# Kernel optimization log

Hardware: AMD Instinct MI355X
Metric: run time of the kernel (lower is better)

The kernel has to match this reference:

```python
import jax, jax.numpy as jnp
import numpy as np

HEADS = 16
EMBED = 1024


def setup_inputs() -> dict:
    key = jax.random.key(0)
    k1, k2, k3, k4, k5, k6 = jax.random.split(key, 6)
    N, S, E = 2, 2048, EMBED
    return {
        "values": jax.random.normal(k1, (N, S, E), dtype=jnp.float32),
        "keys": jax.random.normal(k2, (N, S, E), dtype=jnp.float32),
        "query": jax.random.normal(k3, (N, S, E), dtype=jnp.float32),
        "mask": jax.random.randint(k4, (N, 1, S, S), 0, 2, dtype=jnp.int32),
        "W_out": jax.random.normal(k5, (E, E), dtype=jnp.float32) * 0.02,
        "b_out": jax.random.normal(k6, (E,), dtype=jnp.float32) * 0.02,
    }


def reference(values, keys, query, mask, W_out, b_out):
    N, Q, E = query.shape
    K = keys.shape[1]
    H = HEADS
    D = E // H
    v = values.reshape(N, K, H, D)
    k = keys.reshape(N, K, H, D)
    q = query.reshape(N, Q, H, D)
    # [N, H, Q, K] score matrix (faithful to the naive einsum formulation)
    energy = jnp.einsum("nqhd,nkhd->nhqk", q, k)
    energy = jnp.where(mask == 0, jnp.float32(-1e20), energy)
    # NOTE: original scales by sqrt(embed_size), not sqrt(head_dim)
    attention = jax.nn.softmax(energy / jnp.sqrt(jnp.float32(E)), axis=3)
    out = jnp.einsum("nhqk,nkhd->nqhd", attention, v).reshape(N, Q, E)
    return out @ W_out.T + b_out
```

## Files before the change

kernel.cpp:

```cpp
#include <hip/hip_runtime.h>
#include <hip/hip_bf16.h>


#define S_LEN  2048
#define EMB    1024
#define NHEAD  16
#define DHEAD  64
#define NBATCH 2

#define KSC 0.04508422002778011f

typedef float              f32x4    __attribute__((ext_vector_type(4)));
typedef float              f32x16   __attribute__((ext_vector_type(16)));
typedef __bf16             bf16x8   __attribute__((ext_vector_type(8)));
typedef unsigned short     ushort8v __attribute__((ext_vector_type(8)));
typedef unsigned long long u64;

union FragU { ushort8v u; bf16x8 b; };
union BFrag { unsigned u32[4]; bf16x8 b; };

__device__ __forceinline__ unsigned short f2b(float f) {
  union { __hip_bfloat16 h; unsigned short u; } c;
  c.h = __float2bfloat16(f);
  return c.u;
}

__device__ __forceinline__ unsigned int cvt_pk_bf16(float lo, float hi) {
  unsigned int r;
  asm("v_cvt_pk_bf16_f32 %0, %1, %2" : "=v"(r) : "v"(lo), "v"(hi));
  return r;
}

#define PSWAP(a, b) asm("v_permlane32_swap_b32 %0, %1" : "+v"(a), "+v"(b))

#define GLD16(g, l)                                                            \
  __builtin_amdgcn_global_load_lds(                                            \
      (__attribute__((address_space(1))) void*)(g),                            \
      (__attribute__((address_space(3))) void*)(l), 16, 0, 0)

__global__ __launch_bounds__(256) void prep(
    const float* __restrict__ Wo, unsigned short* __restrict__ Wb,
    const float* __restrict__ Kg, unsigned short* __restrict__ Kb,
    const float* __restrict__ Vg, unsigned short* __restrict__ Vt,
    const int* __restrict__ Mg,   u64* __restrict__ Mb)
{
  const int bid = blockIdx.x;
  const int tid = threadIdx.x;
  if (bid < 2560) {
    const float* X = (bid < 512) ? Wo : Kg;
    unsigned short* Y = (bid < 512) ? Wb : Kb;
    const int bb = (bid < 512) ? bid : bid - 512;
    const size_t i = ((size_t)bb * 256 + tid) * 8;
    float4 a = *reinterpret_cast<const float4*>(X + i);
    float4 b = *reinterpret_cast<const float4*>(X + i + 4);
    ushort8v u;
    u[0] = f2b(a.x); u[1] = f2b(a.y); u[2] = f2b(a.z); u[3] = f2b(a.w);
    u[4] = f2b(b.x); u[5] = f2b(b.y); u[6] = f2b(b.z); u[7] = f2b(b.w);
    *reinterpret_cast<ushort8v*>(Y + i) = u;
  } else if (bid < 3584) {
    __shared__ unsigned short T[64][72];
    const int b2 = bid - 2560;
    const int sb = b2 & 31, h = (b2 >> 5) & 15, n = b2 >> 9;
    const int r = tid >> 2, cb = (tid & 3) * 16;
    const float* src = Vg + ((size_t)(n * S_LEN + sb * 64 + r)) * EMB + h * DHEAD + cb;
    ushort8v u0, u1;
#pragma unroll
    for (int j = 0; j < 2; ++j) {
      float4 x = *reinterpret_cast<const float4*>(src + j * 4);
      u0[j*4+0] = f2b(x.x); u0[j*4+1] = f2b(x.y); u0[j*4+2] = f2b(x.z); u0[j*4+3] = f2b(x.w);
      float4 y = *reinterpret_cast<const float4*>(src + 8 + j * 4);
      u1[j*4+0] = f2b(y.x); u1[j*4+1] = f2b(y.y); u1[j*4+2] = f2b(y.z); u1[j*4+3] = f2b(y.w);
    }
    *reinterpret_cast<ushort8v*>(&T[r][cb])     = u0;
    *reinterpret_cast<ushort8v*>(&T[r][cb + 8]) = u1;
    __syncthreads();
    const int d = tid >> 2, sc_ = (tid & 3) * 16;
    ushort8v o0, o1;
#pragma unroll
    for (int j = 0; j < 8; ++j) { o0[j] = T[sc_ + j][d]; o1[j] = T[sc_ + 8 + j][d]; }
    unsigned short* dst = Vt + ((size_t)((n * NHEAD + h) * DHEAD + d)) * S_LEN + sb * 64 + sc_;
    *reinterpret_cast<ushort8v*>(dst)     = o0;
    *reinterpret_cast<ushort8v*>(dst + 8) = o1;
  } else {
    const int b3 = bid - 3584;
    const size_t base = (size_t)b3 * 1024 + (tid >> 6) * 256;
    const int l = tid & 63;
#pragma unroll
    for (int j = 0; j < 4; ++j) {
      const int v = Mg[base + j * 64 + l];
      u64 bj = __ballot(v != 0);
      if (l == 0) Mb[base / 64 + j] = bj;
    }
  }
}

__global__ __launch_bounds__(512, 4) void attn_fwd(
    const unsigned short* __restrict__ Kb,
    const unsigned short* __restrict__ Vtg,
    const float* __restrict__ Qg,
    const u64* __restrict__ Mbit,
    unsigned short* __restrict__ Og)
{
  __shared__ __attribute__((aligned(16))) char SMEM[65536];

  const int bid = blockIdx.x;
  const int qb = bid & 15, h = (bid >> 4) & 15, n = bid >> 8;
  const int nh = n * NHEAD + h;
  const int tid = threadIdx.x;
  const int w = tid >> 6, sp = w >> 2, wq = w & 3;
  const int l = tid & 63, q5 = l & 31, hi = l >> 5;
  const int hi4 = hi * 4;
  const int q0w = qb * 128 + wq * 32;
  const int qg = q0w + q5;

  FragU qf[4];
  {
    const float* qp = Qg + ((size_t)(n * S_LEN + qg)) * EMB + h * DHEAD + hi * 8;
#pragma unroll
    for (int s = 0; s < 4; ++s) {
      float4 a = *reinterpret_cast<const float4*>(qp + s * 16);
      float4 b = *reinterpret_cast<const float4*>(qp + s * 16 + 4);
      ushort8v u;
      u[0] = f2b(a.x * KSC); u[1] = f2b(a.y * KSC); u[2] = f2b(a.z * KSC); u[3] = f2b(a.w * KSC);
      u[4] = f2b(b.x * KSC); u[5] = f2b(b.y * KSC); u[6] = f2b(b.z * KSC); u[7] = f2b(b.w * KSC);
      qf[s].u = u;
    }
  }

  FragU ones;
#pragma unroll
  for (int j = 0; j < 8; ++j) ones.u[j] = 0x3F80;

  f32x16 acc0 = {}, acc1 = {}, racc = {};

  const int t8 = tid & 255;
  const int srow = t8 >> 3, sc = t8 & 7;
  const char* kbase = (const char*)Kb +
      ((size_t)(n * S_LEN + sp * 1024 + srow)) * 2048 + h * 128 +
      ((sc * 16) ^ ((srow & 7) << 4));
  const char* vbase = (const char*)Vtg +
      ((size_t)(nh * DHEAD + srow)) * 4096 + sp * 2048 +
      ((sc * 16) ^ ((srow & 7) << 4));

  char* Ksp = SMEM + sp * 16384;
  char* Vsp = SMEM + 32768 + sp * 16384;
  const int fsw = (l & 7) << 4;

  const u64* Mq = Mbit + ((size_t)(n * S_LEN + qg)) * 32 + sp * 16;
  u64 mq_cur = Mq[0];

#define ATTN_STAGE(BUF, IT) do {                                               \
    GLD16(kbase + (size_t)(IT) * 131072,          Ksp + (BUF) * 8192 + t8 * 16); \
    GLD16(kbase + (size_t)(IT) * 131072 + 65536,  Ksp + (BUF) * 8192 + 4096 + t8 * 16); \
    GLD16(vbase + (size_t)(IT) * 128,             Vsp + (BUF) * 8192 + t8 * 16); \
    GLD16(vbase + (size_t)(IT) * 128 + 131072,    Vsp + (BUF) * 8192 + 4096 + t8 * 16); \
  } while (0)

#define ATTN_TILE(BUF, IT) do {                                                \
    __syncthreads();                                                           \
    if ((IT) + 1 < 16) ATTN_STAGE((BUF) ^ 1, (IT) + 1);                        \
    const u64 mrow_ = mq_cur;                                                  \
    if ((IT) + 1 < 16) mq_cur = Mq[(IT) + 1];                                  \
    _Pragma("unroll") for (int b = 0; b < 2; ++b) {                            \
      f32x16 Sb = {};                                                          \
      __builtin_amdgcn_s_setprio(1);                                           \
      _Pragma("unroll") for (int s = 0; s < 4; ++s) {                          \
        FragU kf_;                                                             \
        kf_.u = *reinterpret_cast<const ushort8v*>(                            \
            Ksp + (BUF) * 8192 + ((b * 32 + q5) * 128 + ((s * 32 + hi * 16) ^ fsw))); \
        Sb = __builtin_amdgcn_mfma_f32_32x32x16_bf16(kf_.b, qf[s].b, Sb, 0, 0, 0); \
      }                                                                        \
      __builtin_amdgcn_s_setprio(0);                                           \
      const unsigned m32_ = b ? (unsigned)(mrow_ >> 32) : (unsigned)mrow_;     \
      float p_[16];                                                            \
      _Pragma("unroll") for (int t = 0; t < 4; ++t) {                          \
        const unsigned nib_ = m32_ >> (8 * t + hi4);                           \
        _Pragma("unroll") for (int e = 0; e < 4; ++e) {                        \
          const int r = 4 * t + e;                                             \
          float ex_ = __builtin_amdgcn_exp2f(Sb[r]);                           \
          const unsigned sm_ = (unsigned)((int)(nib_ << (31 - e)) >> 31);      \
          p_[r] = __uint_as_float(__float_as_uint(ex_) & sm_);                 \
        }                                                                      \
      }                                                                        \
      unsigned U0 = cvt_pk_bf16(p_[0],  p_[1]),  U1 = cvt_pk_bf16(p_[2],  p_[3]); \
      unsigned U2 = cvt_pk_bf16(p_[4],  p_[5]),  U3 = cvt_pk_bf16(p_[6],  p_[7]); \
      unsigned U4 = cvt_pk_bf16(p_[8],  p_[9]),  U5 = cvt_pk_bf16(p_[10], p_[11]); \
      unsigned U6 = cvt_pk_bf16(p_[12], p_[13]), U7 = cvt_pk_bf16(p_[14], p_[15]); \
      PSWAP(U0, U2); PSWAP(U1, U3); PSWAP(U4, U6); PSWAP(U5, U7);              \
      BFrag F0, F1;                                                            \
      F0.u32[0] = U0; F0.u32[1] = U1; F0.u32[2] = U2; F0.u32[3] = U3;          \
      F1.u32[0] = U4; F1.u32[1] = U5; F1.u32[2] = U6; F1.u32[3] = U7;          \
      __builtin_amdgcn_s_setprio(1);                                           \
      racc = __builtin_amdgcn_mfma_f32_32x32x16_bf16(ones.b, F0.b, racc, 0, 0, 0); \
      racc = __builtin_amdgcn_mfma_f32_32x32x16_bf16(ones.b, F1.b, racc, 0, 0, 0); \
      _Pragma("unroll") for (int db = 0; db < 2; ++db) {                       \
        FragU vf0_, vf1_;                                                      \
        vf0_.u = *reinterpret_cast<const ushort8v*>(                           \
            Vsp + (BUF) * 8192 + ((db * 32 + q5) * 128 + (((2 * b) * 32 + hi * 16) ^ fsw))); \
        vf1_.u = *reinterpret_cast<const ushort8v*>(                           \
            Vsp + (BUF) * 8192 + ((db * 32 + q5) * 128 + (((2 * b + 1) * 32 + hi * 16) ^ fsw))); \
        if (db == 0) {                                                         \
          acc0 = __builtin_amdgcn_mfma_f32_32x32x16_bf16(vf0_.b, F0.b, acc0, 0, 0, 0); \
          acc0 = __builtin_amdgcn_mfma_f32_32x32x16_bf16(vf1_.b, F1.b, acc0, 0, 0, 0); \
        } else {                                                               \
          acc1 = __builtin_amdgcn_mfma_f32_32x32x16_bf16(vf0_.b, F0.b, acc1, 0, 0, 0); \
          acc1 = __builtin_amdgcn_mfma_f32_32x32x16_bf16(vf1_.b, F1.b, acc1, 0, 0, 0); \
        }                                                                      \
      }                                                                        \
      __builtin_amdgcn_s_setprio(0);                                           \
    }                                                                          \
  } while (0)

  ATTN_STAGE(0, 0);
  for (int it = 0; it < 16; it += 2) {
    ATTN_TILE(0, it);
    ATTN_TILE(1, it + 1);
  }

  const float rs = racc[0];
  const int esw = (l & 7) << 4;

  __syncthreads();
  if (sp == 1) {
#pragma unroll
    for (int i = 0; i < 4; ++i) {
      f32x4 v0 = (f32x4){acc0[4*i], acc0[4*i+1], acc0[4*i+2], acc0[4*i+3]};
      f32x4 v1 = (f32x4){acc1[4*i], acc1[4*i+1], acc1[4*i+2], acc1[4*i+3]};
      *reinterpret_cast<f32x4*>(SMEM + wq * 8192 + l * 128 + ((i * 16) ^ esw))      = v0;
      *reinterpret_cast<f32x4*>(SMEM + wq * 8192 + l * 128 + ((64 + i * 16) ^ esw)) = v1;
    }
    *reinterpret_cast<float*>(SMEM + 32768 + wq * 256 + l * 4) = rs;
  }
  __syncthreads();
  if (sp == 0) {
    const float ors = *reinterpret_cast<const float*>(SMEM + 32768 + wq * 256 + l * 4);
    const float rin = 1.0f / (rs + ors);
    unsigned short* orow = Og + ((size_t)(n * S_LEN + qg)) * EMB + h * DHEAD + hi4;
#pragma unroll
    for (int db = 0; db < 2; ++db) {
#pragma unroll
      for (int t = 0; t < 4; ++t) {
        f32x4 pa = *reinterpret_cast<const f32x4*>(
            SMEM + wq * 8192 + l * 128 + ((db * 64 + t * 16) ^ esw));
        float a0, a1, a2, a3;
        if (db == 0) {
          a0 = (acc0[4*t]   + pa[0]) * rin; a1 = (acc0[4*t+1] + pa[1]) * rin;
          a2 = (acc0[4*t+2] + pa[2]) * rin; a3 = (acc0[4*t+3] + pa[3]) * rin;
        } else {
          a0 = (acc1[4*t]   + pa[0]) * rin; a1 = (acc1[4*t+1] + pa[1]) * rin;
          a2 = (acc1[4*t+2] + pa[2]) * rin; a3 = (acc1[4*t+3] + pa[3]) * rin;
        }
        uint2 pk;
        pk.x = cvt_pk_bf16(a0, a1);
        pk.y = cvt_pk_bf16(a2, a3);
        *reinterpret_cast<uint2*>(orow + db * 32 + t * 8) = pk;
      }
    }
  }
}

__global__ __launch_bounds__(256, 2) void out_proj(
    const unsigned short* __restrict__ A,
    const unsigned short* __restrict__ W,
    const float* __restrict__ bias,
    float* __restrict__ Y)
{
  __shared__ __attribute__((aligned(16))) char PSM[65536];

  const int bid = blockIdx.x;
  const int nb = bid & 7, mb = bid >> 3;
  const int tid = threadIdx.x;
  const int w = tid >> 6, wr = w >> 1, wc = w & 1;
  const int l = tid & 63, lg = l >> 4, li = l & 15;
  const int m0 = mb * 128, n0 = nb * 128;

  f32x4 acc[4][4];
#pragma unroll
  for (int mi = 0; mi < 4; ++mi)
#pragma unroll
    for (int ci = 0; ci < 4; ++ci) acc[mi][ci] = (f32x4){0.f, 0.f, 0.f, 0.f};

  const int srow = tid >> 3;
  const int sch  = (tid & 7) * 16;
  const int ssw  = (srow & 7) << 4;
  const char* abase = (const char*)A + ((size_t)(m0 + srow)) * 2048 + (sch ^ ssw);
  const char* bbase = (const char*)W + ((size_t)(n0 + srow)) * 2048 + (sch ^ ssw);
  const int rsw = (li & 7) << 4;

  char* Asm = PSM;
  char* Bsm = PSM + 32768;

#define PROJ_STAGE(BUF, KK) do {                                               \
    _Pragma("unroll") for (int j = 0; j < 4; ++j) {                            \
      GLD16(abase + (size_t)j * 65536 + (KK) * 128,                            \
            Asm + (BUF) * 16384 + j * 4096 + tid * 16);                        \
      GLD16(bbase + (size_t)j * 65536 + (KK) * 128,                            \
            Bsm + (BUF) * 16384 + j * 4096 + tid * 16);                        \
    }                                                                          \
  } while (0)

#define PROJ_TILE(BUF, KK) do {                                                \
    __syncthreads();                                                           \
    if ((KK) + 1 < 16) PROJ_STAGE((BUF) ^ 1, (KK) + 1);                        \
    _Pragma("unroll") for (int s = 0; s < 2; ++s) {                            \
      FragU af_[4], bf_[4];                                                    \
      _Pragma("unroll") for (int mi = 0; mi < 4; ++mi)                         \
        af_[mi].u = *reinterpret_cast<const ushort8v*>(                        \
            Asm + (BUF) * 16384 +                                              \
            ((wr * 64 + mi * 16 + li) * 128 + ((s * 64 + lg * 16) ^ rsw)));    \
      _Pragma("unroll") for (int ci = 0; ci < 4; ++ci)                         \
        bf_[ci].u = *reinterpret_cast<const ushort8v*>(                        \
            Bsm + (BUF) * 16384 +                                              \
            ((wc * 64 + ci * 16 + li) * 128 + ((s * 64 + lg * 16) ^ rsw)));    \
      _Pragma("unroll") for (int mi = 0; mi < 4; ++mi)                         \
        _Pragma("unroll") for (int ci = 0; ci < 4; ++ci)                       \
          acc[mi][ci] = __builtin_amdgcn_mfma_f32_16x16x32_bf16(               \
              af_[mi].b, bf_[ci].b, acc[mi][ci], 0, 0, 0);                     \
    }                                                                          \
  } while (0)

  PROJ_STAGE(0, 0);
  for (int kk = 0; kk < 16; kk += 2) {
    PROJ_TILE(0, kk);
    PROJ_TILE(1, kk + 1);
  }

#pragma unroll
  for (int ci = 0; ci < 4; ++ci) {
    const int col = n0 + wc * 64 + ci * 16 + li;
    const float bv = bias[col];
#pragma unroll
    for (int mi = 0; mi < 4; ++mi) {
#pragma unroll
      for (int r = 0; r < 4; ++r) {
        const int row = m0 + wr * 64 + mi * 16 + lg * 4 + r;
        Y[(size_t)row * EMB + col] = acc[mi][ci][r] + bv;
      }
    }
  }
}

extern "C" void kernel_launch(void* const* d_in, const int* in_sizes, int n_in,
                              void* d_out, int out_size, void* d_ws, size_t ws_size,
                              hipStream_t stream) {
  const float* Vg = (const float*)d_in[0];
  const float* Kg = (const float*)d_in[1];
  const float* Qg = (const float*)d_in[2];
  const int*   Mg = (const int*)d_in[3];
  const float* Wo = (const float*)d_in[4];
  const float* bo = (const float*)d_in[5];
  float* Y = (float*)d_out;

  char* ws = (char*)d_ws;
  unsigned short* Og   = (unsigned short*)(ws);
  unsigned short* Wb   = (unsigned short*)(ws + (8u << 20));
  unsigned short* Kb16 = (unsigned short*)(ws + (10u << 20));
  unsigned short* Vt   = (unsigned short*)(ws + (18u << 20));
  u64*            Mbit = (u64*)(ws + (26u << 20));

  hipLaunchKernelGGL(prep, dim3(11776), dim3(256), 0, stream,
                     Wo, Wb, Kg, Kb16, Vg, Vt, Mg, Mbit);
  hipLaunchKernelGGL(attn_fwd, dim3(NBATCH * NHEAD * (S_LEN / 128)), dim3(512), 0, stream,
                     Kb16, Vt, Qg, Mbit, Og);
  hipLaunchKernelGGL(out_proj, dim3((NBATCH * S_LEN / 128) * (EMB / 128)), dim3(256), 0, stream,
                     Og, Wb, bo, Y);
}
```

Baseline: 87.27 us.

## Triple-buffer 32-key K/V tiles with explicit vmcnt waits and smaller LDS

The attention loop now processes 32-key tiles in place of 64-key tiles. K and V for each tile share one 8 KB buffer, with three buffers in rotation and a prefetch depth of two. The single-barrier sync is replaced by an explicit s_waitcnt vmcnt plus s_barrier, and the V tile gets a narrower swizzle layout. Total LDS drops from 64 KB to 48 KB, which may allow more resident workgroups per CU. The trade-off is twice as many barriers and mask loads per key range, and the mask loads may interact with the vmcnt accounting.

Result: slower. 94.22 us (+8.0%).

```diff
diff --git a/kernel.cpp b/kernel.cpp
--- a/kernel.cpp
+++ b/kernel.cpp
@@ -37,6 +37,9 @@
   __builtin_amdgcn_global_load_lds(                                            \
       (__attribute__((address_space(1))) void*)(g),                            \
       (__attribute__((address_space(3))) void*)(l), 16, 0, 0)
+
+#define WAITVM_(N) asm volatile("s_waitcnt vmcnt(" #N ")" ::: "memory")
+#define WAITVM(N)  WAITVM_(N)
 
 __global__ __launch_bounds__(256) void prep(
     const float* __restrict__ Wo, unsigned short* __restrict__ Wb,
@@ -101,7 +104,7 @@
     const u64* __restrict__ Mbit,
     unsigned short* __restrict__ Og)
 {
-  __shared__ __attribute__((aligned(16))) char SMEM[65536];
+  __shared__ __attribute__((aligned(16))) char SMEM[49152];
 
   const int bid = blockIdx.x;
   const int qb = bid & 15, h = (bid >> 4) & 15, n = bid >> 8;
@@ -134,88 +137,89 @@
   f32x16 acc0 = {}, acc1 = {}, racc = {};
 
   const int t8 = tid & 255;
-  const int srow = t8 >> 3, sc = t8 & 7;
+  const int krow = t8 >> 3, kch = (t8 & 7) * 16;
   const char* kbase = (const char*)Kb +
-      ((size_t)(n * S_LEN + sp * 1024 + srow)) * 2048 + h * 128 +
-      ((sc * 16) ^ ((srow & 7) << 4));
+      ((size_t)(n * S_LEN + sp * 1024 + krow)) * 2048 + h * 128 +
+      (kch ^ ((krow & 7) << 4));
+  const int vrow = t8 >> 2, vch = (t8 & 3) * 16;
   const char* vbase = (const char*)Vtg +
-      ((size_t)(nh * DHEAD + srow)) * 4096 + sp * 2048 +
-      ((sc * 16) ^ ((srow & 7) << 4));
-
-  char* Ksp = SMEM + sp * 16384;
-  char* Vsp = SMEM + 32768 + sp * 16384;
-  const int fsw = (l & 7) << 4;
-
-  const u64* Mq = Mbit + ((size_t)(n * S_LEN + qg)) * 32 + sp * 16;
-  u64 mq_cur = Mq[0];
+      ((size_t)(nh * DHEAD + vrow)) * 4096 + sp * 2048 +
+      (vch ^ ((vrow & 3) << 4));
+
+  char* Ksp = SMEM + sp * 24576;
+  const int fsw  = (l & 7) << 4;
+  const int vfsw = (l & 3) << 4;
+
+  const unsigned* Mq32 = reinterpret_cast<const unsigned*>(
+      Mbit + ((size_t)(n * S_LEN + qg)) * 32 + sp * 16);
 
 #define ATTN_STAGE(BUF, IT) do {                                               \
-    GLD16(kbase + (size_t)(IT) * 131072,          Ksp + (BUF) * 8192 + t8 * 16); \
-    GLD16(kbase + (size_t)(IT) * 131072 + 65536,  Ksp + (BUF) * 8192 + 4096 + t8 * 16); \
-    GLD16(vbase + (size_t)(IT) * 128,             Vsp + (BUF) * 8192 + t8 * 16); \
-    GLD16(vbase + (size_t)(IT) * 128 + 131072,    Vsp + (BUF) * 8192 + 4096 + t8 * 16); \
+    GLD16(kbase + (size_t)(IT) * 65536, Ksp + (BUF) * 8192 + t8 * 16);         \
+    GLD16(vbase + (size_t)(IT) * 64,    Ksp + (BUF) * 8192 + 4096 + t8 * 16);  \
   } while (0)
 
-#define ATTN_TILE(BUF, IT) do {                                                \
-    __syncthreads();                                                           \
-    if ((IT) + 1 < 16) ATTN_STAGE((BUF) ^ 1, (IT) + 1);                        \
-    const u64 mrow_ = mq_cur;                                                  \
-    if ((IT) + 1 < 16) mq_cur = Mq[(IT) + 1];                                  \
-    _Pragma("unroll") for (int b = 0; b < 2; ++b) {                            \
-      f32x16 Sb = {};                                                          \
-      __builtin_amdgcn_s_setprio(1);                                           \
-      _Pragma("unroll") for (int s = 0; s < 4; ++s) {                          \
-        FragU kf_;                                                             \
-        kf_.u = *reinterpret_cast<const ushort8v*>(                            \
-            Ksp + (BUF) * 8192 + ((b * 32 + q5) * 128 + ((s * 32 + hi * 16) ^ fsw))); \
-        Sb = __builtin_amdgcn_mfma_f32_32x32x16_bf16(kf_.b, qf[s].b, Sb, 0, 0, 0); \
+#define ATTN_TILE(BUF, IT, WAITN, NBUF, DOSTAGE) do {                          \
+    WAITVM(WAITN);                                 \
+    __builtin_amdgcn_s_barrier();                  \
+    asm volatile("" ::: "memory");                                             \
+    if (DOSTAGE) ATTN_STAGE(NBUF, (IT) + 2);       \
+    const unsigned m32_ = Mq32[(IT)];                                          \
+    f32x16 Sb = {};                                                            \
+    __builtin_amdgcn_s_setprio(1);                                             \
+    _Pragma("unroll") for (int s = 0; s < 4; ++s) {                            \
+      FragU kf_;                                                               \
+      kf_.u = *reinterpret_cast<const ushort8v*>(                              \
+          Ksp + (BUF) * 8192 + (q5 * 128 + ((s * 32 + hi * 16) ^ fsw)));       \
+      Sb = __builtin_amdgcn_mfma_f32_32x32x16_bf16(kf_.b, qf[s].b, Sb, 0, 0, 0); \
+    }                                                                          \
+    __builtin_amdgcn_s_setprio(0);                                             \
+    float p_[16];                                                              \
+    _Pragma("unroll") for (int t = 0; t < 4; ++t) {                            \
+      const unsigned nib_ = m32_ >> (8 * t + hi4);                             \
+      _Pragma("unroll") for (int e = 0; e < 4; ++e) {                          \
+        const int r = 4 * t + e;                                               \
+        float ex_ = __builtin_amdgcn_exp2f(Sb[r]);                             \
+        const unsigned sm_ = (unsigned)((int)(nib_ << (31 - e)) >> 31);        \
+        p_[r] = __uint_as_float(__float_as_uint(ex_) & sm_);                   \
       }                                                                        \
-      __builtin_amdgcn_s_setprio(0);                                           \
-      const unsigned m32_ = b ? (unsigned)(mrow_ >> 32) : (unsigned)mrow_;     \
-      float p_[16];                                                            \
-      _Pragma("unroll") for (int t = 0; t < 4; ++t) {                          \
-        const unsigned nib_ = m32_ >> (8 * t + hi4);                           \
-        _Pragma("unroll") for (int e = 0; e < 4; ++e) {                        \
-          const int r = 4 * t + e;                                             \
-          float ex_ = __builtin_amdgcn_exp2f(Sb[r]);                           \
-          const unsigned sm_ = (unsigned)((int)(nib_ << (31 - e)) >> 31);      \
-          p_[r] = __uint_as_float(__float_as_uint(ex_) & sm_);                 \
-        }                                                                      \
+    }                                                                          \
+    unsigned U0 = cvt_pk_bf16(p_[0],  p_[1]),  U1 = cvt_pk_bf16(p_[2],  p_[3]); \
+    unsigned U2 = cvt_pk_bf16(p_[4],  p_[5]),  U3 = cvt_pk_bf16(p_[6],  p_[7]); \
+    unsigned U4 = cvt_pk_bf16(p_[8],  p_[9]),  U5 = cvt_pk_bf16(p_[10], p_[11]); \
+    unsigned U6 = cvt_pk_bf16(p_[12], p_[13]), U7 = cvt_pk_bf16(p_[14], p_[15]); \
+    PSWAP(U0, U2); PSWAP(U1, U3); PSWAP(U4, U6); PSWAP(U5, U7);                \
+    BFrag F0, F1;                                                              \
+    F0.u32[0] = U0; F0.u32[1] = U1; F0.u32[2] = U2; F0.u32[3] = U3;            \
+    F1.u32[0] = U4; F1.u32[1] = U5; F1.u32[2] = U6; F1.u32[3] = U7;            \
+    __builtin_amdgcn_s_setprio(1);                                             \
+    racc = __builtin_amdgcn_mfma_f32_32x32x16_bf16(ones.b, F0.b, racc, 0, 0, 0); \
+    racc = __builtin_amdgcn_mfma_f32_32x32x16_bf16(ones.b, F1.b, racc, 0, 0, 0); \
+    _Pragma("unroll") for (int db = 0; db < 2; ++db) {                         \
+      FragU vf0_, vf1_;                                                        \
+      vf0_.u = *reinterpret_cast<const ushort8v*>(                             \
+          Ksp + (BUF) * 8192 + 4096 + ((db * 32 + q5) * 64 + ((0  + hi * 16) ^ vfsw))); \
+      vf1_.u = *reinterpret_cast<const ushort8v*>(                             \
+          Ksp + (BUF) * 8192 + 4096 + ((db * 32 + q5) * 64 + ((32 + hi * 16) ^ vfsw))); \
+      if (db == 0) {                                                           \
+        acc0 = __builtin_amdgcn_mfma_f32_32x32x16_bf16(vf0_.b, F0.b, acc0, 0, 0, 0); \
+        acc0 = __builtin_amdgcn_mfma_f32_32x32x16_bf16(vf1_.b, F1.b, acc0, 0, 0, 0); \
+      } else {                                                                 \
+        acc1 = __builtin_amdgcn_mfma_f32_32x32x16_bf16(vf0_.b, F0.b, acc1, 0, 0, 0); \
+        acc1 = __builtin_amdgcn_mfma_f32_32x32x16_bf16(vf1_.b, F1.b, acc1, 0, 0, 0); \
       }                                                                        \
-      unsigned U0 = cvt_pk_bf16(p_[0],  p_[1]),  U1 = cvt_pk_bf16(p_[2],  p_[3]); \
-      unsigned U2 = cvt_pk_bf16(p_[4],  p_[5]),  U3 = cvt_pk_bf16(p_[6],  p_[7]); \
-      unsigned U4 = cvt_pk_bf16(p_[8],  p_[9]),  U5 = cvt_pk_bf16(p_[10], p_[11]); \
-      unsigned U6 = cvt_pk_bf16(p_[12], p_[13]), U7 = cvt_pk_bf16(p_[14], p_[15]); \
-      PSWAP(U0, U2); PSWAP(U1, U3); PSWAP(U4, U6); PSWAP(U5, U7);              \
-      BFrag F0, F1;                                                            \
-      F0.u32[0] = U0; F0.u32[1] = U1; F0.u32[2] = U2; F0.u32[3] = U3;          \
-      F1.u32[0] = U4; F1.u32[1] = U5; F1.u32[2] = U6; F1.u32[3] = U7;          \
-      __builtin_amdgcn_s_setprio(1);                                           \
-      racc = __builtin_amdgcn_mfma_f32_32x32x16_bf16(ones.b, F0.b, racc, 0, 0, 0); \
-      racc = __builtin_amdgcn_mfma_f32_32x32x16_bf16(ones.b, F1.b, racc, 0, 0, 0); \
-      _Pragma("unroll") for (int db = 0; db < 2; ++db) {                       \
-        FragU vf0_, vf1_;                                                      \
-        vf0_.u = *reinterpret_cast<const ushort8v*>(                           \
-            Vsp + (BUF) * 8192 + ((db * 32 + q5) * 128 + (((2 * b) * 32 + hi * 16) ^ fsw))); \
-        vf1_.u = *reinterpret_cast<const ushort8v*>(                           \
-            Vsp + (BUF) * 8192 + ((db * 32 + q5) * 128 + (((2 * b + 1) * 32 + hi * 16) ^ fsw))); \
-        if (db == 0) {                                                         \
-          acc0 = __builtin_amdgcn_mfma_f32_32x32x16_bf16(vf0_.b, F0.b, acc0, 0, 0, 0); \
-          acc0 = __builtin_amdgcn_mfma_f32_32x32x16_bf16(vf1_.b, F1.b, acc0, 0, 0, 0); \
-        } else {                                                               \
-          acc1 = __builtin_amdgcn_mfma_f32_32x32x16_bf16(vf0_.b, F0.b, acc1, 0, 0, 0); \
-          acc1 = __builtin_amdgcn_mfma_f32_32x32x16_bf16(vf1_.b, F1.b, acc1, 0, 0, 0); \
-        }                                                                      \
-      }                                                                        \
-      __builtin_amdgcn_s_setprio(0);                                           \
-    }                                                                          \
+    }                                                                          \
+    __builtin_amdgcn_s_setprio(0);                                             \
   } while (0)
 
   ATTN_STAGE(0, 0);
-  for (int it = 0; it < 16; it += 2) {
-    ATTN_TILE(0, it);
-    ATTN_TILE(1, it + 1);
-  }
+  ATTN_STAGE(1, 1);
+  for (int it = 0; it < 30; it += 3) {
+    ATTN_TILE(0, it,     2, 2, 1);
+    ATTN_TILE(1, it + 1, 2, 0, 1);
+    ATTN_TILE(2, it + 2, 2, 1, 1);
+  }
+  ATTN_TILE(0, 30, 2, 0, 0);
+  ATTN_TILE(1, 31, 0, 0, 0);
 
   const float rs = racc[0];
   const int esw = (l & 7) << 4;
```
